# Performance work log

Measured on AMD Instinct MI355X. Metric: run time of the kernel, lower is better.

The kernel has to match this reference:

```python
import jax, jax.numpy as jnp
import numpy as np

N = 4096   # support size
B = 512    # number of histograms (columns)


def setup_inputs() -> dict:
    key = jax.random.key(0)
    kU, kP, kK = jax.random.split(key, 3)
    # u must satisfy u < lamda; uniform [0,1) with lamda=10 is safe.
    U = jax.random.uniform(kU, (N, B), dtype=jnp.float32)
    # strictly positive histograms (avoid log(0))
    P = jax.random.uniform(kP, (N, B), dtype=jnp.float32) + 0.01
    # positive Gibbs kernel
    K = jax.random.uniform(kK, (N, N), dtype=jnp.float32) + 1e-3
    return {"U": U, "P": P, "K": K, "eps": 1, "lamda": 10}


def reference(U, P, K, eps, lamda):
    """Vectorized OTModel.OT_unbal: sum over columns of the primal unbalanced OT
    value reconstructed from dual potential U.  gamma_ij = a_i * K_ij * f_j is
    never materialized; all reductions over gamma are contracted analytically.
    """
    eps = jnp.float32(eps)
    lamda = jnp.float32(lamda)
    # f in log domain: (lamda/eps) * log(lamda/(lamda-u))          [N, B]
    flog = (lamda / eps) * jnp.log(lamda / (lamda - U))
    f = jnp.exp(flog)
    # alpha/eps with the mean-scale stabilization from get_alpha_unbal
    scale = flog.mean(axis=0)                                      # [B]
    KF_stab = K @ jnp.exp(flog - scale)                            # [N, B]
    alpha_over_eps = jnp.log(P) - (jnp.log(KF_stab) + scale)       # [N, B]
    a = jnp.exp(alpha_over_eps)                                    # exp(alpha/eps)
    Kf = K @ f                                                     # [N, B]
    # (gamma @ flog).sum() = sum_i a_i * (K @ (f * flog))_i
    term1 = jnp.sum(a * (K @ (f * flog)))
    # (gamma.T @ (alpha/eps)).sum() = sum_i a_i * (alpha/eps)_i * (K @ f)_i
    term2 = jnp.sum(a * alpha_over_eps * Kf)
    # gamma.sum()
    term3 = jnp.sum(a * Kf)
    # gamma.sum(0)_j = f_j * (K^T @ a)_j
    gcol = f * (K.T @ a)                                           # [N, B]
    # q from get_q_unbal (unstabilized, as in the original)
    q = (lamda / (lamda - U)) ** (lamda / eps + 1.0) * (K.T @ (P / Kf))
    # KL(a,b) = sum(a*log(a/b) - a)   (inputs strictly positive here)
    kl = jnp.sum(gcol * jnp.log(gcol / q) - gcol)
    return eps * (term1 + term2 - term3) + lamda * kl
```

## Files before the change

### kernel.cpp

```cpp
#include <hip/hip_runtime.h>

#define NN 4096
#define BB 512

typedef __attribute__((ext_vector_type(4))) float f32x4;
typedef __attribute__((ext_vector_type(16))) float f32x16;
typedef __attribute__((ext_vector_type(4))) int i32x4;
typedef __attribute__((ext_vector_type(8))) int i32x8;
typedef unsigned short ushort;
typedef unsigned char uchar;
typedef unsigned int uint;
typedef __attribute__((ext_vector_type(4))) ushort ushort4v;

#define ASCALE 16384.0f
#define AINV   6.103515625e-05f
#define SCL1   0x7f7f7f7f

__device__ __forceinline__ float scal_val(const void* p) {
    int b = *(const int*)p;
    if (b >= 1 && b <= 1000000) return (float)b;
    return __int_as_float(b);
}

__device__ __forceinline__ ushort f2bf(float x) {
    unsigned u = __float_as_uint(x);
    u += 0x7fffu + ((u >> 16) & 1u);
    return (ushort)(u >> 16);
}
__device__ __forceinline__ float bf2f(ushort b) {
    return __uint_as_float((uint)b << 16);
}

__device__ __forceinline__ uint pack4_fp8(float a, float b, float c, float d) {
    int v = __builtin_amdgcn_cvt_pk_fp8_f32(a, b, 0, false);
    v = __builtin_amdgcn_cvt_pk_fp8_f32(c, d, v, true);
    return (uint)v;
}

__device__ __forceinline__ void gload16(const void* g, void* l) {
    __builtin_amdgcn_global_load_lds(
        (const __attribute__((address_space(1))) unsigned int*)g,
        (__attribute__((address_space(3))) unsigned int*)l, 16, 0, 0);
}

__device__ __forceinline__ double wave_sum(double v) {
#pragma unroll
    for (int s = 32; s > 0; s >>= 1) v += __shfl_down(v, s, 64);
    return v;
}

__device__ __forceinline__ int offA(int i, int k) {
    return (((i >> 7) * 64 + (k >> 6)) << 13) + ((i & 127) << 6) +
           ((((k >> 4) & 3) ^ ((i >> 1) & 3)) << 4) + (k & 15);
}
__device__ __forceinline__ int offB(int j, int k) {
    return (((j >> 6) * 64 + (k >> 6)) << 12) + ((j & 63) << 6) +
           ((((k >> 4) & 3) ^ ((j >> 1) & 3)) << 4) + (k & 15);
}

__device__ __forceinline__ i32x8 frag64(const uchar* rowbase, int u0byte) {
    i32x4 lo = *(const i32x4*)(rowbase + u0byte);
    i32x4 hi = *(const i32x4*)(rowbase + (u0byte ^ 16));
    i32x8 r;
    r[0] = lo[0]; r[1] = lo[1]; r[2] = lo[2]; r[3] = lo[3];
    r[4] = hi[0]; r[5] = hi[1]; r[6] = hi[2]; r[7] = hi[3];
    return r;
}


__device__ __forceinline__ void gemm_decode(int bid, int& kh, int& i0, int& j0) {
    const int xcd = bid & 7, slot = bid >> 3;
    const int p = xcd * 16 + (slot >> 3);
    kh = p & 3;
    i0 = (p >> 2) * 128;
    j0 = (slot & 7) * 64;
}

__global__ __launch_bounds__(256) void k_prep(const float* __restrict__ K,
                                              const float* __restrict__ U,
                                              uchar* __restrict__ Kb,
                                              uchar* __restrict__ KTb,
                                              uchar* __restrict__ fT,
                                              const void* epsp, const void* lamp,
                                              double* __restrict__ parts) {
    __shared__ float tile[64][65];
    const int t = threadIdx.x;
    const int tx = t & 15, ty = t >> 4;
    const int bid = blockIdx.x;

    if (bid == 0 && t == 0) *(unsigned int*)(parts + 3072) = 0u;

    if (bid < 4096) {
        const int c0 = (bid & 63) * 64, r0 = (bid >> 6) * 64;
#pragma unroll
        for (int it = 0; it < 4; ++it) {
            int row = ty + it * 16;
            int i = r0 + row;
            float4 v = *(const float4*)&K[(size_t)i * NN + c0 + tx * 4];
            *(uint*)&Kb[offA(i, c0 + tx * 4)] = pack4_fp8(v.x, v.y, v.z, v.w);
            tile[row][tx * 4 + 0] = v.x;
            tile[row][tx * 4 + 1] = v.y;
            tile[row][tx * 4 + 2] = v.z;
            tile[row][tx * 4 + 3] = v.w;
        }
        __syncthreads();
#pragma unroll
        for (int it = 0; it < 4; ++it) {
            int row = ty + it * 16;
            int i = c0 + row;
            int k = r0 + tx * 4;
            *(uint*)&KTb[offA(i, k)] =
                pack4_fp8(tile[tx * 4 + 0][row], tile[tx * 4 + 1][row],
                          tile[tx * 4 + 2][row], tile[tx * 4 + 3][row]);
        }
    } else {
        const int r = bid - 4096;
        const int c0 = (r & 7) * 64;
        const int r0 = (r >> 3) * 64;
        const float eps = scal_val(epsp), lam = scal_val(lamp);
        const float rr = lam / eps;
#pragma unroll
        for (int it = 0; it < 4; ++it) {
            int row = ty + it * 16;
            float4 v = *(const float4*)&U[(size_t)(r0 + row) * BB + c0 + tx * 4];
            float uu[4] = {v.x, v.y, v.z, v.w};
#pragma unroll
            for (int k = 0; k < 4; ++k) {
                float L = __logf(lam / (lam - uu[k]));
                tile[row][tx * 4 + k] = __expf(rr * L);
            }
        }
        __syncthreads();
#pragma unroll
        for (int it = 0; it < 4; ++it) {
            int row = ty + it * 16;
            int j = c0 + row;
            int k = r0 + tx * 4;
            *(uint*)&fT[offB(j, k)] =
                pack4_fp8(tile[tx * 4 + 0][row], tile[tx * 4 + 1][row],
                          tile[tx * 4 + 2][row], tile[tx * 4 + 3][row]);
        }
    }
}

__global__ __launch_bounds__(256) void k_gemm1(const uchar* __restrict__ Kb,
                                               const uchar* __restrict__ fT,
                                               ushort* __restrict__ Y1b) {
    __shared__ __align__(16) uchar As[3][128 * 64];
    __shared__ __align__(16) uchar Bf[3][64 * 64];

    const int tid = threadIdx.x;
    const int lane = tid & 63;
    const int w = tid >> 6;
    int kh, i0, j0;
    gemm_decode(blockIdx.x, kh, i0, j0);
    const int h = lane >> 5;
    const int r = lane & 31;
    const int u0b = (((h << 1) ^ ((r >> 1) & 3)) << 4);

    f32x16 acc0 = {}, acc1 = {};

    const uchar* apanel = Kb + ((size_t)(i0 >> 7) << 19);
    const uchar* bpanel = fT + ((size_t)(j0 >> 6) << 18);

    auto stage = [&](int ks, int b) {
        const uchar* ga = apanel + ((size_t)ks << 13) + w * 2048 + lane * 16;
        gload16(ga, &As[b][w * 2048]);
        gload16(ga + 1024, &As[b][w * 2048 + 1024]);
        const uchar* gb = bpanel + ((size_t)ks << 12) + w * 1024 + lane * 16;
        gload16(gb, &Bf[b][w * 1024]);
    };

    const int ks0 = kh * 16;
    stage(ks0, 0);
    stage(ks0 + 1, 1);
    int cur = 0, pf = 2;
    for (int step = 0; step < 16; ++step) {
        if (step < 15) asm volatile("s_waitcnt vmcnt(3)" ::: "memory");
        else           asm volatile("s_waitcnt vmcnt(0)" ::: "memory");
        __builtin_amdgcn_s_barrier();
        __builtin_amdgcn_sched_barrier(0);
        if (step < 14) stage(ks0 + step + 2, pf);
        i32x8 av = frag64(&As[cur][(w * 32 + r) << 6], u0b);
        i32x8 bv0 = frag64(&Bf[cur][r << 6], u0b);
        i32x8 bv1 = frag64(&Bf[cur][(32 + r) << 6], u0b);
        acc0 = __builtin_amdgcn_mfma_scale_f32_32x32x64_f8f6f4(
            av, bv0, acc0, 0, 0, 0, SCL1, 0, SCL1);
        acc1 = __builtin_amdgcn_mfma_scale_f32_32x32x64_f8f6f4(
            av, bv1, acc1, 0, 0, 0, SCL1, 0, SCL1);
        __builtin_amdgcn_sched_barrier(0);
        cur = (cur == 2) ? 0 : cur + 1;
        pf = (pf == 2) ? 0 : pf + 1;
    }

    ushort* o1 = Y1b + (size_t)kh * NN * BB;
#pragma unroll
    for (int reg = 0; reg < 16; ++reg) {
        const int row = i0 + w * 32 + (reg & 3) + 8 * (reg >> 2) + 4 * h;
        o1[(size_t)row * BB + j0 + r] = f2bf(acc0[reg]);
        o1[(size_t)row * BB + j0 + 32 + r] = f2bf(acc1[reg]);
    }
}

__global__ __launch_bounds__(256) void k_epi(const ushort* __restrict__ Y1b,
                                             const float* __restrict__ P,
                                             uchar* __restrict__ aT,
                                             double* __restrict__ parts) {
    __shared__ float ta[64][65];
    __shared__ double bred[4][2];
    const int t = threadIdx.x;
    const int lane = t & 63;
    const int w = t >> 6;
    const int tx = t & 15, ty = t >> 4;
    const int j0 = blockIdx.x * 64;
    const int i0 = blockIdx.y * 64;
    const int bid = blockIdx.y * 8 + blockIdx.x;
    const size_t H = (size_t)NN * BB;

    double t2 = 0.0, t3 = 0.0;
#pragma unroll
    for (int it = 0; it < 4; ++it) {
        int row = ty + it * 16;
        size_t off = (size_t)(i0 + row) * BB + j0 + tx * 4;
        ushort4v q0 = *(const ushort4v*)(Y1b + off);
        ushort4v q1 = *(const ushort4v*)(Y1b + H + off);
        ushort4v q2 = *(const ushort4v*)(Y1b + 2 * H + off);
        ushort4v q3 = *(const ushort4v*)(Y1b + 3 * H + off);
        float4 p4 = *(const float4*)(P + off);
        float pv[4] = {p4.x, p4.y, p4.z, p4.w};
#pragma unroll
        for (int e = 0; e < 4; ++e) {
            float y1 = bf2f(q0[e]) + bf2f(q1[e]) + bf2f(q2[e]) + bf2f(q3[e]);
            float aij = pv[e] / y1;
            t2 += (double)(pv[e] * __logf(aij));
            t3 += (double)pv[e];
            ta[row][tx * 4 + e] = aij * ASCALE;
        }
    }
    __syncthreads();
#pragma unroll
    for (int it = 0; it < 4; ++it) {
        int row = ty + it * 16;
        int j = j0 + row;
        *(uint*)&aT[offB(j, i0 + tx * 4)] =
            pack4_fp8(ta[tx * 4 + 0][row], ta[tx * 4 + 1][row],
                      ta[tx * 4 + 2][row], ta[tx * 4 + 3][row]);
    }

    t2 = wave_sum(t2); t3 = wave_sum(t3);
    if (lane == 0) { bred[w][0] = t2; bred[w][1] = t3; }
    __syncthreads();
    if (t == 0) {
        double b = 0, c = 0;
#pragma unroll
        for (int ww = 0; ww < 4; ++ww) { b += bred[ww][0]; c += bred[ww][1]; }
        parts[2048 + bid] = b;
        parts[2560 + bid] = c;
    }
}

__global__ __launch_bounds__(256) void k_gemm2(const uchar* __restrict__ KTb,
                                               const uchar* __restrict__ aT,
                                               const float* __restrict__ U,
                                               const void* epsp, const void* lamp,
                                               double* __restrict__ parts,
                                               float* __restrict__ out) {
    __shared__ __align__(16) uchar As[3][128 * 64];
    __shared__ __align__(16) uchar Bs[3][64 * 64];
    __shared__ double bred[4][4];
    __shared__ int lastflag;

    const float eps = scal_val(epsp), lam = scal_val(lamp);
    const float rr = lam / eps;
    const int tid = threadIdx.x;
    const int lane = tid & 63;
    const int w = tid >> 6;
    const int bid = blockIdx.x;
    int kh, i0, j0;
    gemm_decode(bid, kh, i0, j0);
    const int h = lane >> 5;
    const int r = lane & 31;
    const int u0b = (((h << 1) ^ ((r >> 1) & 3)) << 4);

    f32x16 acc0 = {}, acc1 = {};

    const uchar* apanel = KTb + ((size_t)(i0 >> 7) << 19);
    const uchar* bpanel = aT + ((size_t)(j0 >> 6) << 18);

    auto stage = [&](int ks, int b) {
        const uchar* ga = apanel + ((size_t)ks << 13) + w * 2048 + lane * 16;
        gload16(ga, &As[b][w * 2048]);
        gload16(ga + 1024, &As[b][w * 2048 + 1024]);
        const uchar* gb = bpanel + ((size_t)ks << 12) + w * 1024 + lane * 16;
        gload16(gb, &Bs[b][w * 1024]);
    };

    const int ks0 = kh * 16;
    stage(ks0, 0);
    stage(ks0 + 1, 1);
    int cur = 0, pf = 2;
    for (int step = 0; step < 16; ++step) {
        if (step < 15) asm volatile("s_waitcnt vmcnt(3)" ::: "memory");
        else           asm volatile("s_waitcnt vmcnt(0)" ::: "memory");
        __builtin_amdgcn_s_barrier();
        __builtin_amdgcn_sched_barrier(0);
        if (step < 14) stage(ks0 + step + 2, pf);
        i32x8 av = frag64(&As[cur][(w * 32 + r) << 6], u0b);
        i32x8 bv0 = frag64(&Bs[cur][r << 6], u0b);
        i32x8 bv1 = frag64(&Bs[cur][(32 + r) << 6], u0b);
        acc0 = __builtin_amdgcn_mfma_scale_f32_32x32x64_f8f6f4(
            av, bv0, acc0, 0, 0, 0, SCL1, 0, SCL1);
        acc1 = __builtin_amdgcn_mfma_scale_f32_32x32x64_f8f6f4(
            av, bv1, acc1, 0, 0, 0, SCL1, 0, SCL1);
        __builtin_amdgcn_sched_barrier(0);
        cur = (cur == 2) ? 0 : cur + 1;
        pf = (pf == 2) ? 0 : pf + 1;
    }

    double t1p = 0.0, klp = 0.0;
#pragma unroll
    for (int reg = 0; reg < 16; ++reg) {
        const int ib = i0 + w * 32 + (reg & 3) + 8 * (reg >> 2) + 4 * h;
#pragma unroll
        for (int nt = 0; nt < 2; ++nt) {
            const int j = j0 + nt * 32 + r;
            float s = (nt ? acc1[reg] : acc0[reg]) * AINV;
            float u = U[(size_t)ib * BB + j];
            float L = __logf(lam / (lam - u));
            float fv = __expf(rr * L);
            t1p += (double)(fv * rr * L * s);
            klp -= (double)(fv * (1.0f + L) * s);
        }
    }

    t1p = wave_sum(t1p); klp = wave_sum(klp);
    if (lane == 0) { bred[w][0] = t1p; bred[w][1] = klp; }
    __syncthreads();
    if (tid == 0) {
        double a = 0, b = 0;
#pragma unroll
        for (int ww = 0; ww < 4; ++ww) { a += bred[ww][0]; b += bred[ww][1]; }
        parts[bid] = a;
        parts[1024 + bid] = b;
        __threadfence();
        uint old = atomicAdd((unsigned int*)(parts + 3072), 1u);
        lastflag = (old == 1023) ? 1 : 0;
    }
    __syncthreads();

    if (lastflag) {
        __threadfence();
        const volatile double* vp = parts;
        double s0 = 0.0, s1 = 0.0, s2 = 0.0, s3 = 0.0;
        for (int i = tid; i < 1024; i += 256) {
            s0 += vp[i];
            s1 += vp[1024 + i];
        }
        for (int i = tid; i < 512; i += 256) {
            s2 += vp[2048 + i];
            s3 += vp[2560 + i];
        }
        s0 = wave_sum(s0); s1 = wave_sum(s1);
        s2 = wave_sum(s2); s3 = wave_sum(s3);
        if (lane == 0) {
            bred[w][0] = s0; bred[w][1] = s1; bred[w][2] = s2; bred[w][3] = s3;
        }
        __syncthreads();
        if (tid == 0) {
            double t1 = 0, kl = 0, t2 = 0, t3 = 0;
#pragma unroll
            for (int ww = 0; ww < 4; ++ww) {
                t1 += bred[ww][0]; kl += bred[ww][1];
                t2 += bred[ww][2]; t3 += bred[ww][3];
            }
            out[0] = (float)((double)eps * (t1 + t2 - t3) + (double)lam * kl);
        }
    }
}

extern "C" void kernel_launch(void* const* d_in, const int* in_sizes, int n_in,
                              void* d_out, int out_size, void* d_ws, size_t ws_size,
                              hipStream_t stream) {
    const float* U = (const float*)d_in[0];
    const float* P = (const float*)d_in[1];
    const float* K = (const float*)d_in[2];
    const void* epsp = d_in[3];
    const void* lamp = d_in[4];

    double* parts = (double*)d_ws;
    char* base = (char*)d_ws + (64 << 10);
    uchar* Kb   = (uchar*)base;
    uchar* KTb  = (uchar*)(base + ((size_t)16 << 20));
    uchar* fT   = (uchar*)(base + ((size_t)32 << 20));
    uchar* aT   = (uchar*)(base + ((size_t)34 << 20));
    ushort* Y1b = (ushort*)(base + ((size_t)36 << 20));

    k_prep<<<4608, 256, 0, stream>>>(K, U, Kb, KTb, fT, epsp, lamp, parts);
    k_gemm1<<<1024, 256, 0, stream>>>(Kb, fT, Y1b);
    k_epi<<<dim3(8, 64), 256, 0, stream>>>(Y1b, P, aT, parts);
    k_gemm2<<<1024, 256, 0, stream>>>(KTb, aT, U, epsp, lamp, parts, (float*)d_out);
}
```

Measured before the change: 175.3 us.

## Fuse epilogue into gemm1 via last-arriving split-K block; widen prep stores

```diff
diff --git a/kernel.cpp b/kernel.cpp
--- a/kernel.cpp
+++ b/kernel.cpp
@@ -10,7 +10,7 @@
 typedef unsigned short ushort;
 typedef unsigned char uchar;
 typedef unsigned int uint;
-typedef __attribute__((ext_vector_type(4))) ushort ushort4v;
+typedef unsigned long long u64;
 
 #define ASCALE 16384.0f
 #define AINV   6.103515625e-05f
@@ -47,6 +47,14 @@
 #pragma unroll
     for (int s = 32; s > 0; s >>= 1) v += __shfl_down(v, s, 64);
     return v;
+}
+
+__device__ __forceinline__ void ld4bf_vol(const ushort* p, float* o) {
+    u64 v = *(const volatile u64*)p;
+    o[0] = bf2f((ushort)v);
+    o[1] = bf2f((ushort)(v >> 16));
+    o[2] = bf2f((ushort)(v >> 32));
+    o[3] = bf2f((ushort)(v >> 48));
 }
 
 __device__ __forceinline__ int offA(int i, int k) {
@@ -67,14 +75,6 @@
     return r;
 }
 
-
-__device__ __forceinline__ void gemm_decode(int bid, int& kh, int& i0, int& j0) {
-    const int xcd = bid & 7, slot = bid >> 3;
-    const int p = xcd * 16 + (slot >> 3);
-    kh = p & 3;
-    i0 = (p >> 2) * 128;
-    j0 = (slot & 7) * 64;
-}
 
 __global__ __launch_bounds__(256) void k_prep(const float* __restrict__ K,
                                               const float* __restrict__ U,
@@ -85,75 +85,89 @@
                                               double* __restrict__ parts) {
     __shared__ float tile[64][65];
     const int t = threadIdx.x;
-    const int tx = t & 15, ty = t >> 4;
+    const int row = t >> 2;
+    const int q = t & 3;
     const int bid = blockIdx.x;
 
-    if (bid == 0 && t == 0) *(unsigned int*)(parts + 3072) = 0u;
+    if (t == 0 && bid < 257) ((uint*)(parts + 3072))[bid] = 0u;
 
     if (bid < 4096) {
         const int c0 = (bid & 63) * 64, r0 = (bid >> 6) * 64;
-#pragma unroll
-        for (int it = 0; it < 4; ++it) {
-            int row = ty + it * 16;
-            int i = r0 + row;
-            float4 v = *(const float4*)&K[(size_t)i * NN + c0 + tx * 4];
-            *(uint*)&Kb[offA(i, c0 + tx * 4)] = pack4_fp8(v.x, v.y, v.z, v.w);
-            tile[row][tx * 4 + 0] = v.x;
-            tile[row][tx * 4 + 1] = v.y;
-            tile[row][tx * 4 + 2] = v.z;
-            tile[row][tx * 4 + 3] = v.w;
-        }
+        const int i = r0 + row;
+        const float* src = &K[(size_t)i * NN + c0 + q * 16];
+        float4 a0 = *(const float4*)(src);
+        float4 a1 = *(const float4*)(src + 4);
+        float4 a2 = *(const float4*)(src + 8);
+        float4 a3 = *(const float4*)(src + 12);
+        i32x4 pk;
+        pk[0] = (int)pack4_fp8(a0.x, a0.y, a0.z, a0.w);
+        pk[1] = (int)pack4_fp8(a1.x, a1.y, a1.z, a1.w);
+        pk[2] = (int)pack4_fp8(a2.x, a2.y, a2.z, a2.w);
+        pk[3] = (int)pack4_fp8(a3.x, a3.y, a3.z, a3.w);
+        *(i32x4*)&Kb[offA(i, c0 + q * 16)] = pk;
+        float vv[16] = {a0.x, a0.y, a0.z, a0.w, a1.x, a1.y, a1.z, a1.w,
+                        a2.x, a2.y, a2.z, a2.w, a3.x, a3.y, a3.z, a3.w};
+#pragma unroll
+        for (int e = 0; e < 16; ++e) tile[row][q * 16 + e] = vv[e];
         __syncthreads();
-#pragma unroll
-        for (int it = 0; it < 4; ++it) {
-            int row = ty + it * 16;
-            int i = c0 + row;
-            int k = r0 + tx * 4;
-            *(uint*)&KTb[offA(i, k)] =
-                pack4_fp8(tile[tx * 4 + 0][row], tile[tx * 4 + 1][row],
-                          tile[tx * 4 + 2][row], tile[tx * 4 + 3][row]);
-        }
+        float b[16];
+#pragma unroll
+        for (int e = 0; e < 16; ++e) b[e] = tile[q * 16 + e][row];
+        i32x4 pk2;
+        pk2[0] = (int)pack4_fp8(b[0], b[1], b[2], b[3]);
+        pk2[1] = (int)pack4_fp8(b[4], b[5], b[6], b[7]);
+        pk2[2] = (int)pack4_fp8(b[8], b[9], b[10], b[11]);
+        pk2[3] = (int)pack4_fp8(b[12], b[13], b[14], b[15]);
+        *(i32x4*)&KTb[offA(c0 + row, r0 + q * 16)] = pk2;
     } else {
-        const int r = bid - 4096;
-        const int c0 = (r & 7) * 64;
-        const int r0 = (r >> 3) * 64;
+        const int rb = bid - 4096;
+        const int c0 = (rb & 7) * 64;
+        const int r0 = (rb >> 3) * 64;
         const float eps = scal_val(epsp), lam = scal_val(lamp);
         const float rr = lam / eps;
-#pragma unroll
-        for (int it = 0; it < 4; ++it) {
-            int row = ty + it * 16;
-            float4 v = *(const float4*)&U[(size_t)(r0 + row) * BB + c0 + tx * 4];
-            float uu[4] = {v.x, v.y, v.z, v.w};
-#pragma unroll
-            for (int k = 0; k < 4; ++k) {
-                float L = __logf(lam / (lam - uu[k]));
-                tile[row][tx * 4 + k] = __expf(rr * L);
-            }
+        const float* src = &U[(size_t)(r0 + row) * BB + c0 + q * 16];
+        float4 a0 = *(const float4*)(src);
+        float4 a1 = *(const float4*)(src + 4);
+        float4 a2 = *(const float4*)(src + 8);
+        float4 a3 = *(const float4*)(src + 12);
+        float uu[16] = {a0.x, a0.y, a0.z, a0.w, a1.x, a1.y, a1.z, a1.w,
+                        a2.x, a2.y, a2.z, a2.w, a3.x, a3.y, a3.z, a3.w};
+#pragma unroll
+        for (int e = 0; e < 16; ++e) {
+            float L = __logf(lam / (lam - uu[e]));
+            tile[row][q * 16 + e] = __expf(rr * L);
         }
         __syncthreads();
-#pragma unroll
-        for (int it = 0; it < 4; ++it) {
-            int row = ty + it * 16;
-            int j = c0 + row;
-            int k = r0 + tx * 4;
-            *(uint*)&fT[offB(j, k)] =
-                pack4_fp8(tile[tx * 4 + 0][row], tile[tx * 4 + 1][row],
-                          tile[tx * 4 + 2][row], tile[tx * 4 + 3][row]);
-        }
+        float b[16];
+#pragma unroll
+        for (int e = 0; e < 16; ++e) b[e] = tile[q * 16 + e][row];
+        i32x4 pk2;
+        pk2[0] = (int)pack4_fp8(b[0], b[1], b[2], b[3]);
+        pk2[1] = (int)pack4_fp8(b[4], b[5], b[6], b[7]);
+        pk2[2] = (int)pack4_fp8(b[8], b[9], b[10], b[11]);
+        pk2[3] = (int)pack4_fp8(b[12], b[13], b[14], b[15]);
+        *(i32x4*)&fT[offB(c0 + row, r0 + q * 16)] = pk2;
     }
 }
 
 __global__ __launch_bounds__(256) void k_gemm1(const uchar* __restrict__ Kb,
                                                const uchar* __restrict__ fT,
-                                               ushort* __restrict__ Y1b) {
+                                               const float* __restrict__ P,
+                                               ushort* __restrict__ Y1b,
+                                               uchar* __restrict__ aT,
+                                               double* __restrict__ parts) {
     __shared__ __align__(16) uchar As[3][128 * 64];
     __shared__ __align__(16) uchar Bf[3][64 * 64];
+    __shared__ double bred[4][2];
+    __shared__ int lastf;
 
     const int tid = threadIdx.x;
     const int lane = tid & 63;
     const int w = tid >> 6;
-    int kh, i0, j0;
-    gemm_decode(blockIdx.x, kh, i0, j0);
+    const int bid = blockIdx.x;
+    const int kh = bid & 3;
+    const int i0 = ((bid >> 2) & 31) * 128;
+    const int j0 = (bid >> 7) * 64;
     const int h = lane >> 5;
     const int r = lane & 31;
     const int u0b = (((h << 1) ^ ((r >> 1) & 3)) << 4);
@@ -200,62 +214,66 @@
         o1[(size_t)row * BB + j0 + r] = f2bf(acc0[reg]);
         o1[(size_t)row * BB + j0 + 32 + r] = f2bf(acc1[reg]);
     }
-}
-
-__global__ __launch_bounds__(256) void k_epi(const ushort* __restrict__ Y1b,
-                                             const float* __restrict__ P,
-                                             uchar* __restrict__ aT,
-                                             double* __restrict__ parts) {
-    __shared__ float ta[64][65];
-    __shared__ double bred[4][2];
-    const int t = threadIdx.x;
-    const int lane = t & 63;
-    const int w = t >> 6;
-    const int tx = t & 15, ty = t >> 4;
-    const int j0 = blockIdx.x * 64;
-    const int i0 = blockIdx.y * 64;
-    const int bid = blockIdx.y * 8 + blockIdx.x;
+
+    __threadfence();
+    __syncthreads();
+    const int tile_id = ((i0 >> 7) << 3) | (j0 >> 6);
+    if (tid == 0) {
+        uint old = atomicAdd(((uint*)(parts + 3072)) + tile_id, 1u);
+        lastf = (old == 3) ? 1 : 0;
+    }
+    __syncthreads();
+    if (!lastf) return;
+    __threadfence();
+
+    float (*ta)[65] = (float(*)[65])(&As[0][0]);
+    const int tx = tid & 15, ty = tid >> 4;
     const size_t H = (size_t)NN * BB;
-
     double t2 = 0.0, t3 = 0.0;
 #pragma unroll
-    for (int it = 0; it < 4; ++it) {
-        int row = ty + it * 16;
-        size_t off = (size_t)(i0 + row) * BB + j0 + tx * 4;
-        ushort4v q0 = *(const ushort4v*)(Y1b + off);
-        ushort4v q1 = *(const ushort4v*)(Y1b + H + off);
-        ushort4v q2 = *(const ushort4v*)(Y1b + 2 * H + off);
-        ushort4v q3 = *(const ushort4v*)(Y1b + 3 * H + off);
-        float4 p4 = *(const float4*)(P + off);
-        float pv[4] = {p4.x, p4.y, p4.z, p4.w};
-#pragma unroll
-        for (int e = 0; e < 4; ++e) {
-            float y1 = bf2f(q0[e]) + bf2f(q1[e]) + bf2f(q2[e]) + bf2f(q3[e]);
-            float aij = pv[e] / y1;
-            t2 += (double)(pv[e] * __logf(aij));
-            t3 += (double)pv[e];
-            ta[row][tx * 4 + e] = aij * ASCALE;
-        }
-    }
-    __syncthreads();
-#pragma unroll
-    for (int it = 0; it < 4; ++it) {
-        int row = ty + it * 16;
-        int j = j0 + row;
-        *(uint*)&aT[offB(j, i0 + tx * 4)] =
-            pack4_fp8(ta[tx * 4 + 0][row], ta[tx * 4 + 1][row],
-                      ta[tx * 4 + 2][row], ta[tx * 4 + 3][row]);
+    for (int p = 0; p < 2; ++p) {
+        const int i0e = i0 + p * 64;
+        if (p) __syncthreads();
+#pragma unroll
+        for (int it = 0; it < 4; ++it) {
+            int rw = ty + it * 16;
+            size_t off = (size_t)(i0e + rw) * BB + j0 + tx * 4;
+            float y0[4], y1v[4], y2[4], y3[4];
+            ld4bf_vol(Y1b + off, y0);
+            ld4bf_vol(Y1b + H + off, y1v);
+            ld4bf_vol(Y1b + 2 * H + off, y2);
+            ld4bf_vol(Y1b + 3 * H + off, y3);
+            float4 p4 = *(const float4*)(P + off);
+            float pv[4] = {p4.x, p4.y, p4.z, p4.w};
+#pragma unroll
+            for (int e = 0; e < 4; ++e) {
+                float ys = y0[e] + y1v[e] + y2[e] + y3[e];
+                float aij = pv[e] / ys;
+                t2 += (double)(pv[e] * __logf(aij));
+                t3 += (double)pv[e];
+                ta[rw][tx * 4 + e] = aij * ASCALE;
+            }
+        }
+        __syncthreads();
+#pragma unroll
+        for (int it = 0; it < 4; ++it) {
+            int rw = ty + it * 16;
+            int j = j0 + rw;
+            *(uint*)&aT[offB(j, i0e + tx * 4)] =
+                pack4_fp8(ta[tx * 4 + 0][rw], ta[tx * 4 + 1][rw],
+                          ta[tx * 4 + 2][rw], ta[tx * 4 + 3][rw]);
+        }
     }
 
     t2 = wave_sum(t2); t3 = wave_sum(t3);
     if (lane == 0) { bred[w][0] = t2; bred[w][1] = t3; }
     __syncthreads();
-    if (t == 0) {
+    if (tid == 0) {
         double b = 0, c = 0;
 #pragma unroll
         for (int ww = 0; ww < 4; ++ww) { b += bred[ww][0]; c += bred[ww][1]; }
-        parts[2048 + bid] = b;
-        parts[2560 + bid] = c;
+        parts[2048 + tile_id] = b;
+        parts[2560 + tile_id] = c;
     }
 }
 
@@ -276,8 +294,9 @@
     const int lane = tid & 63;
     const int w = tid >> 6;
     const int bid = blockIdx.x;
-    int kh, i0, j0;
-    gemm_decode(bid, kh, i0, j0);
+    const int kh = bid & 3;
+    const int i0 = ((bid >> 2) & 31) * 128;
+    const int j0 = (bid >> 7) * 64;
     const int h = lane >> 5;
     const int r = lane & 31;
     const int u0b = (((h << 1) ^ ((r >> 1) & 3)) << 4);
@@ -343,7 +362,7 @@
         parts[bid] = a;
         parts[1024 + bid] = b;
         __threadfence();
-        uint old = atomicAdd((unsigned int*)(parts + 3072), 1u);
+        uint old = atomicAdd(((uint*)(parts + 3072)) + 256, 1u);
         lastflag = (old == 1023) ? 1 : 0;
     }
     __syncthreads();
@@ -356,10 +375,8 @@
             s0 += vp[i];
             s1 += vp[1024 + i];
         }
-        for (int i = tid; i < 512; i += 256) {
-            s2 += vp[2048 + i];
-            s3 += vp[2560 + i];
-        }
+        s2 = vp[2048 + tid];
+        s3 = vp[2560 + tid];
         s0 = wave_sum(s0); s1 = wave_sum(s1);
         s2 = wave_sum(s2); s3 = wave_sum(s3);
         if (lane == 0) {
@@ -396,7 +413,6 @@
     ushort* Y1b = (ushort*)(base + ((size_t)36 << 20));
 
     k_prep<<<4608, 256, 0, stream>>>(K, U, Kb, KTb, fT, epsp, lamp, parts);
-    k_gemm1<<<1024, 256, 0, stream>>>(Kb, fT, Y1b);
-    k_epi<<<dim3(8, 64), 256, 0, stream>>>(Y1b, P, aT, parts);
+    k_gemm1<<<1024, 256, 0, stream>>>(Kb, fT, P, Y1b, aT, parts);
     k_gemm2<<<1024, 256, 0, stream>>>(KTb, aT, U, epsp, lamp, parts, (float*)d_out);
 }
```

New measurement: 340.8 us. +94.5%, slower.
